# Optimization experiments

Measured on AMD Instinct MI355X. Metric: run time of the kernel, lower is better.

The kernel has to match this reference:

```python
import jax, jax.numpy as jnp
import numpy as np

N_NODES = 2_000_000
N_EDGES = 16_777_216
N_REL = 4


def setup_inputs() -> dict:
    key = jax.random.key(0)
    ks = jax.random.split(key, 13)
    inp = {
        "author_x": jax.random.normal(ks[0], (N_NODES, 4), jnp.float32),
        "paper_x": jax.random.normal(ks[1], (N_NODES, 4), jnp.float32),
        "src_index": jax.random.randint(ks[2], (N_EDGES,), 0, N_NODES, jnp.int64 if jax.config.jax_enable_x64 else jnp.int32).astype(jnp.int32),
        "dst_index": jax.random.randint(ks[3], (N_EDGES,), 0, N_NODES).astype(jnp.int32),
        "edge_type_index": jax.random.randint(ks[4], (N_EDGES,), 0, N_REL).astype(jnp.int32),
        "edge_src_is_paper": jax.random.randint(ks[5], (N_REL,), 0, 2).astype(jnp.int32),
        "edge_dst_is_paper": jax.random.randint(ks[6], (N_REL,), 0, 2).astype(jnp.int32),
        "Wa": jax.random.normal(ks[7], (4, 4), jnp.float32) * 0.5,
        "ba": jax.random.normal(ks[8], (4,), jnp.float32) * 0.1,
        "Wp": jax.random.normal(ks[9], (4, 4), jnp.float32) * 0.5,
        "bp": jax.random.normal(ks[10], (4,), jnp.float32) * 0.1,
        "Ws": jax.random.normal(ks[11], (8,), jnp.float32) * 0.5,
        "bs": jax.random.normal(ks[12], (1,), jnp.float32) * 0.1,
    }
    return inp


def reference(author_x, paper_x, src_index, dst_index, edge_type_index,
              edge_src_is_paper, edge_dst_is_paper, Wa, ba, Wp, bp, Ws, bs):
    # Encode node tables (tiny GEMMs): [N,4] @ [4,4]^T + [4]
    author_h = author_x @ Wa.T + ba
    paper_h = paper_x @ Wp.T + bp
    # Per-edge relation-type dispatch: 1 = paper table, 0 = author table
    src_p = edge_src_is_paper[edge_type_index].astype(bool)  # [E]
    dst_p = edge_dst_is_paper[edge_type_index].astype(bool)  # [E]
    src_repr = jnp.where(src_p[:, None], paper_h[src_index], author_h[src_index])  # [E,4]
    dst_repr = jnp.where(dst_p[:, None], paper_h[dst_index], author_h[dst_index])  # [E,4]
    # scorer: Linear(8,1) on concat, squeeze last dim -> [E]
    logits = jnp.concatenate([src_repr, dst_repr], axis=-1) @ Ws + bs[0]
    return logits
```

## Files before the change

kernel.cpp:

```cpp
#include <hip/hip_runtime.h>

typedef int         iv4 __attribute__((ext_vector_type(4)));
typedef float       fv4 __attribute__((ext_vector_type(4)));
typedef _Float16    hv4 __attribute__((ext_vector_type(4)));

struct Fold {
    float va_s[4], va_d[4], vp_s[4], vp_d[4];
    float ca_s, ca_d, cp_s, cp_d;
};

__device__ inline Fold make_fold(const float* __restrict__ Wa, const float* __restrict__ ba,
                                 const float* __restrict__ Wp, const float* __restrict__ bp,
                                 const float* __restrict__ Ws) {
    Fold f;
    float w0 = Ws[0], w1 = Ws[1], w2 = Ws[2], w3 = Ws[3];
    float w4 = Ws[4], w5 = Ws[5], w6 = Ws[6], w7 = Ws[7];
#pragma unroll
    for (int j = 0; j < 4; ++j) {
        f.va_s[j] = w0*Wa[j] + w1*Wa[4+j] + w2*Wa[8+j] + w3*Wa[12+j];
        f.va_d[j] = w4*Wa[j] + w5*Wa[4+j] + w6*Wa[8+j] + w7*Wa[12+j];
        f.vp_s[j] = w0*Wp[j] + w1*Wp[4+j] + w2*Wp[8+j] + w3*Wp[12+j];
        f.vp_d[j] = w4*Wp[j] + w5*Wp[4+j] + w6*Wp[8+j] + w7*Wp[12+j];
    }
    f.ca_s = w0*ba[0] + w1*ba[1] + w2*ba[2] + w3*ba[3];
    f.ca_d = w4*ba[0] + w5*ba[1] + w6*ba[2] + w7*ba[3];
    f.cp_s = w0*bp[0] + w1*bp[1] + w2*bp[2] + w3*bp[3];
    f.cp_d = w4*bp[0] + w5*bp[1] + w6*bp[2] + w7*bp[3];
    return f;
}

__device__ inline void node_scores(const Fold& f, fv4 a, fv4 p,
                                   float& as, float& ps, float& ad, float& pd) {
    as = a.x*f.va_s[0] + a.y*f.va_s[1] + a.z*f.va_s[2] + a.w*f.va_s[3] + f.ca_s;
    ad = a.x*f.va_d[0] + a.y*f.va_d[1] + a.z*f.va_d[2] + a.w*f.va_d[3] + f.ca_d;
    ps = p.x*f.vp_s[0] + p.y*f.vp_s[1] + p.z*f.vp_s[2] + p.w*f.vp_s[3] + f.cp_s;
    pd = p.x*f.vp_d[0] + p.y*f.vp_d[1] + p.z*f.vp_d[2] + p.w*f.vp_d[3] + f.cp_d;
}

__global__ __launch_bounds__(256) void node_pass1(
    const fv4* __restrict__ ax, const fv4* __restrict__ px,
    const float* __restrict__ Wa, const float* __restrict__ ba,
    const float* __restrict__ Wp, const float* __restrict__ bp,
    const float* __restrict__ Ws,
    hv4* __restrict__ sc, unsigned* __restrict__ maxes, int n)
{
    Fold f = make_fold(Wa, ba, Wp, bp, Ws);
    float ms = 0.f, md = 0.f;
    int stride = gridDim.x * blockDim.x;
    for (int i = blockIdx.x * blockDim.x + threadIdx.x; i < n; i += stride) {
        fv4 a = __builtin_nontemporal_load(ax + i);
        fv4 p = __builtin_nontemporal_load(px + i);
        float as, ps, ad, pd;
        node_scores(f, a, p, as, ps, ad, pd);
        hv4 h;
        h.x = (_Float16)as; h.y = (_Float16)ps; h.z = (_Float16)ad; h.w = (_Float16)pd;
        sc[i] = h;
        ms = fmaxf(ms, fmaxf(fabsf(as), fabsf(ps)));
        md = fmaxf(md, fmaxf(fabsf(ad), fabsf(pd)));
    }
#pragma unroll
    for (int off = 32; off >= 1; off >>= 1) {
        ms = fmaxf(ms, __shfl_down(ms, off));
        md = fmaxf(md, __shfl_down(md, off));
    }
    __shared__ float lms[4], lmd[4];
    int wave = threadIdx.x >> 6, lane = threadIdx.x & 63;
    if (lane == 0) { lms[wave] = ms; lmd[wave] = md; }
    __syncthreads();
    if (threadIdx.x == 0) {
        float bms = fmaxf(fmaxf(lms[0], lms[1]), fmaxf(lms[2], lms[3]));
        float bmd = fmaxf(fmaxf(lmd[0], lmd[1]), fmaxf(lmd[2], lmd[3]));
        atomicMax(&maxes[0], __float_as_uint(bms));
        atomicMax(&maxes[1], __float_as_uint(bmd));
    }
}

__global__ __launch_bounds__(256) void node_pass2(
    const hv4* __restrict__ sc, const unsigned* __restrict__ maxes,
    unsigned long long* __restrict__ ts8, unsigned long long* __restrict__ td8, int n4)
{
    int i = blockIdx.x * blockDim.x + threadIdx.x;
    if (i >= n4) return;
    float inv_s = 127.f / fmaxf(__uint_as_float(maxes[0]), 1e-20f);
    float inv_d = 127.f / fmaxf(__uint_as_float(maxes[1]), 1e-20f);
    unsigned long long vs = 0, vd = 0;
#pragma unroll
    for (int j = 0; j < 4; ++j) {
        hv4 h = sc[4*i + j];
        int qas = min(127, max(-127, __float2int_rn((float)h.x * inv_s)));
        int qps = min(127, max(-127, __float2int_rn((float)h.y * inv_s)));
        int qad = min(127, max(-127, __float2int_rn((float)h.z * inv_d)));
        int qpd = min(127, max(-127, __float2int_rn((float)h.w * inv_d)));
        vs |= (unsigned long long)((unsigned)qas & 0xffu) << (16*j);
        vs |= (unsigned long long)((unsigned)qps & 0xffu) << (16*j + 8);
        vd |= (unsigned long long)((unsigned)qad & 0xffu) << (16*j);
        vd |= (unsigned long long)((unsigned)qpd & 0xffu) << (16*j + 8);
    }
    ts8[i] = vs;
    td8[i] = vd;
}

__global__ __launch_bounds__(256) void edge_src_pass(
    const iv4* __restrict__ src4, const iv4* __restrict__ et4,
    const int* __restrict__ esp, const int* __restrict__ edp,
    const signed char* __restrict__ ts,
    unsigned long long* __restrict__ qsrc,
    unsigned char* __restrict__ dbits, int n8)
{
    int i = blockIdx.x * blockDim.x + threadIdx.x;
    if (i >= n8) return;
    unsigned smask = (unsigned)((esp[0]&1) | ((esp[1]&1)<<1) | ((esp[2]&1)<<2) | ((esp[3]&1)<<3));
    unsigned dmask = (unsigned)((edp[0]&1) | ((edp[1]&1)<<1) | ((edp[2]&1)<<2) | ((edp[3]&1)<<3));

    iv4 s0 = __builtin_nontemporal_load(src4 + 2*i);
    iv4 s1 = __builtin_nontemporal_load(src4 + 2*i + 1);
    iv4 t0 = __builtin_nontemporal_load(et4 + 2*i);
    iv4 t1 = __builtin_nontemporal_load(et4 + 2*i + 1);
    int ty[8] = { t0.x&3, t0.y&3, t0.z&3, t0.w&3, t1.x&3, t1.y&3, t1.z&3, t1.w&3 };
    int sx[8] = { s0.x, s0.y, s0.z, s0.w, s1.x, s1.y, s1.z, s1.w };

    int a[8];
#pragma unroll
    for (int k = 0; k < 8; ++k) a[k] = 2*sx[k] + (int)((smask >> ty[k]) & 1u);

    int q[8];
#pragma unroll
    for (int k = 0; k < 8; ++k) q[k] = (int)ts[a[k]];

    unsigned long long o = 0;
    unsigned db = 0;
#pragma unroll
    for (int k = 0; k < 8; ++k) {
        o |= (unsigned long long)((unsigned)q[k] & 0xffu) << (8*k);
        db |= ((dmask >> ty[k]) & 1u) << k;
    }
    __builtin_nontemporal_store(o, qsrc + i);
    __builtin_nontemporal_store((unsigned char)db, dbits + i);
}

__global__ __launch_bounds__(256) void edge_dst_pass(
    const iv4* __restrict__ dst4,
    const unsigned char* __restrict__ dbits,
    const float* __restrict__ bs, const unsigned* __restrict__ maxes,
    const signed char* __restrict__ td,
    const unsigned long long* __restrict__ qsrc,
    fv4* __restrict__ out4, int n8)
{
    int i = blockIdx.x * blockDim.x + threadIdx.x;
    if (i >= n8) return;
    float b = bs[0];
    float scale_s = __uint_as_float(maxes[0]) * (1.f / 127.f);
    float scale_d = __uint_as_float(maxes[1]) * (1.f / 127.f);

    iv4 d0 = __builtin_nontemporal_load(dst4 + 2*i);
    iv4 d1 = __builtin_nontemporal_load(dst4 + 2*i + 1);
    unsigned db = (unsigned)dbits[i];
    unsigned long long qq = qsrc[i];
    int dx[8] = { d0.x, d0.y, d0.z, d0.w, d1.x, d1.y, d1.z, d1.w };

    int a[8];
#pragma unroll
    for (int k = 0; k < 8; ++k) a[k] = 2*dx[k] + (int)((db >> k) & 1u);

    int qd[8];
#pragma unroll
    for (int k = 0; k < 8; ++k) qd[k] = (int)td[a[k]];

    float r[8];
#pragma unroll
    for (int k = 0; k < 8; ++k) {
        int qs = (int)(signed char)((qq >> (8*k)) & 0xffull);
        r[k] = (float)qs * scale_s + (float)qd[k] * scale_d + b;
    }
    fv4 o0, o1;
    o0.x = r[0]; o0.y = r[1]; o0.z = r[2]; o0.w = r[3];
    o1.x = r[4]; o1.y = r[5]; o1.z = r[6]; o1.w = r[7];
    __builtin_nontemporal_store(o0, out4 + 2*i);
    __builtin_nontemporal_store(o1, out4 + 2*i + 1);
}

__global__ __launch_bounds__(256) void fused_kernel(
    const fv4* __restrict__ ax, const fv4* __restrict__ px,
    const int* __restrict__ src, const int* __restrict__ dst, const int* __restrict__ et,
    const int* __restrict__ esp, const int* __restrict__ edp,
    const float* __restrict__ Wa, const float* __restrict__ ba,
    const float* __restrict__ Wp, const float* __restrict__ bp,
    const float* __restrict__ Ws, const float* __restrict__ bs,
    float* __restrict__ out, int n)
{
    int e = blockIdx.x * blockDim.x + threadIdx.x;
    if (e >= n) return;
    Fold f = make_fold(Wa, ba, Wp, bp, Ws);
    int t = et[e];
    int sp = esp[t] & 1, dp = edp[t] & 1;
    fv4 sv = sp ? px[src[e]] : ax[src[e]];
    fv4 dv = dp ? px[dst[e]] : ax[dst[e]];
    float ssc = sp ? (sv.x*f.vp_s[0] + sv.y*f.vp_s[1] + sv.z*f.vp_s[2] + sv.w*f.vp_s[3] + f.cp_s)
                   : (sv.x*f.va_s[0] + sv.y*f.va_s[1] + sv.z*f.va_s[2] + sv.w*f.va_s[3] + f.ca_s);
    float dsc = dp ? (dv.x*f.vp_d[0] + dv.y*f.vp_d[1] + dv.z*f.vp_d[2] + dv.w*f.vp_d[3] + f.cp_d)
                   : (dv.x*f.va_d[0] + dv.y*f.va_d[1] + dv.z*f.va_d[2] + dv.w*f.va_d[3] + f.ca_d);
    out[e] = ssc + dsc + bs[0];
}

extern "C" void kernel_launch(void* const* d_in, const int* in_sizes, int n_in,
                              void* d_out, int out_size, void* d_ws, size_t ws_size,
                              hipStream_t stream) {
    const float* ax  = (const float*)d_in[0];
    const float* px  = (const float*)d_in[1];
    const int*   src = (const int*)d_in[2];
    const int*   dst = (const int*)d_in[3];
    const int*   et  = (const int*)d_in[4];
    const int*   esp = (const int*)d_in[5];
    const int*   edp = (const int*)d_in[6];
    const float* Wa  = (const float*)d_in[7];
    const float* ba  = (const float*)d_in[8];
    const float* Wp  = (const float*)d_in[9];
    const float* bp  = (const float*)d_in[10];
    const float* Ws  = (const float*)d_in[11];
    const float* bs  = (const float*)d_in[12];
    float* out = (float*)d_out;

    const int n_nodes = in_sizes[0] / 4;
    const int n_edges = in_sizes[2];

    auto rnd = [](size_t v) { return (v + 255) & ~(size_t)255; };
    size_t union_sz = rnd((size_t)n_edges > (size_t)n_nodes * 8 ? (size_t)n_edges
                                                                : (size_t)n_nodes * 8);
    const size_t off_u  = 256;
    const size_t off_ts = off_u + union_sz;
    const size_t off_td = off_ts + rnd((size_t)n_nodes * 2);
    const size_t off_db = off_td + rnd((size_t)n_nodes * 2);
    const size_t need   = off_db + rnd((size_t)(n_edges / 8) + 1);

    if (ws_size >= need && (n_edges & 7) == 0 && (n_nodes & 3) == 0) {
        unsigned* maxes = (unsigned*)d_ws;
        hv4* sc = (hv4*)((char*)d_ws + off_u);
        unsigned long long* qsrc = (unsigned long long*)((char*)d_ws + off_u);
        signed char* ts = (signed char*)((char*)d_ws + off_ts);
        signed char* td = (signed char*)((char*)d_ws + off_td);
        unsigned char* dbits = (unsigned char*)((char*)d_ws + off_db);

        (void)hipMemsetAsync(maxes, 0, 2 * sizeof(unsigned), stream);
        node_pass1<<<2048, 256, 0, stream>>>(
            (const fv4*)ax, (const fv4*)px, Wa, ba, Wp, bp, Ws, sc, maxes, n_nodes);
        const int n4 = n_nodes / 4;
        node_pass2<<<(n4 + 255) / 256, 256, 0, stream>>>(
            sc, maxes, (unsigned long long*)ts, (unsigned long long*)td, n4);

        const int n8 = n_edges / 8;
        const int nb = (n8 + 255) / 256;
        edge_src_pass<<<nb, 256, 0, stream>>>(
            (const iv4*)src, (const iv4*)et, esp, edp, ts, qsrc, dbits, n8);
        edge_dst_pass<<<nb, 256, 0, stream>>>(
            (const iv4*)dst, dbits, bs, maxes, td, qsrc, (fv4*)out, n8);
    } else {
        fused_kernel<<<(n_edges + 255) / 256, 256, 0, stream>>>(
            (const fv4*)ax, (const fv4*)px, src, dst, et, esp, edp,
            Wa, ba, Wp, bp, Ws, bs, out, n_edges);
    }
}
```

Before: 460.1 us.

## Recompute node scores in pass2 instead of staging fp16 intermediates; drop atomics and memset

Pass1 now only computes per-block abs-max values and writes them to a small array, with no fp16 score buffer. Pass2 reduces those block maxima inside every block and recomputes the node scores from the raw inputs before quantizing. This removes the 16 MB fp16 write and read, the memset launch and the global atomics. In exchange the 64 MB node input is read twice, and every pass2 block redundantly reduces 2048 partial maxima.

```diff
diff --git a/kernel.cpp b/kernel.cpp
--- a/kernel.cpp
+++ b/kernel.cpp
@@ -2,7 +2,6 @@
 
 typedef int         iv4 __attribute__((ext_vector_type(4)));
 typedef float       fv4 __attribute__((ext_vector_type(4)));
-typedef _Float16    hv4 __attribute__((ext_vector_type(4)));
 
 struct Fold {
     float va_s[4], va_d[4], vp_s[4], vp_d[4];
@@ -37,24 +36,23 @@
     pd = p.x*f.vp_d[0] + p.y*f.vp_d[1] + p.z*f.vp_d[2] + p.w*f.vp_d[3] + f.cp_d;
 }
 
+#define P1_BLOCKS 2048
+
 __global__ __launch_bounds__(256) void node_pass1(
     const fv4* __restrict__ ax, const fv4* __restrict__ px,
     const float* __restrict__ Wa, const float* __restrict__ ba,
     const float* __restrict__ Wp, const float* __restrict__ bp,
     const float* __restrict__ Ws,
-    hv4* __restrict__ sc, unsigned* __restrict__ maxes, int n)
+    float* __restrict__ bms, float* __restrict__ bmd, int n)
 {
     Fold f = make_fold(Wa, ba, Wp, bp, Ws);
     float ms = 0.f, md = 0.f;
     int stride = gridDim.x * blockDim.x;
     for (int i = blockIdx.x * blockDim.x + threadIdx.x; i < n; i += stride) {
-        fv4 a = __builtin_nontemporal_load(ax + i);
-        fv4 p = __builtin_nontemporal_load(px + i);
+        fv4 a = ax[i];
+        fv4 p = px[i];
         float as, ps, ad, pd;
         node_scores(f, a, p, as, ps, ad, pd);
-        hv4 h;
-        h.x = (_Float16)as; h.y = (_Float16)ps; h.z = (_Float16)ad; h.w = (_Float16)pd;
-        sc[i] = h;
         ms = fmaxf(ms, fmaxf(fabsf(as), fabsf(ps)));
         md = fmaxf(md, fmaxf(fabsf(ad), fabsf(pd)));
     }
@@ -68,29 +66,58 @@
     if (lane == 0) { lms[wave] = ms; lmd[wave] = md; }
     __syncthreads();
     if (threadIdx.x == 0) {
-        float bms = fmaxf(fmaxf(lms[0], lms[1]), fmaxf(lms[2], lms[3]));
-        float bmd = fmaxf(fmaxf(lmd[0], lmd[1]), fmaxf(lmd[2], lmd[3]));
-        atomicMax(&maxes[0], __float_as_uint(bms));
-        atomicMax(&maxes[1], __float_as_uint(bmd));
+        bms[blockIdx.x] = fmaxf(fmaxf(lms[0], lms[1]), fmaxf(lms[2], lms[3]));
+        bmd[blockIdx.x] = fmaxf(fmaxf(lmd[0], lmd[1]), fmaxf(lmd[2], lmd[3]));
     }
 }
 
 __global__ __launch_bounds__(256) void node_pass2(
-    const hv4* __restrict__ sc, const unsigned* __restrict__ maxes,
+    const fv4* __restrict__ ax, const fv4* __restrict__ px,
+    const float* __restrict__ Wa, const float* __restrict__ ba,
+    const float* __restrict__ Wp, const float* __restrict__ bp,
+    const float* __restrict__ Ws,
+    const float* __restrict__ bms, const float* __restrict__ bmd, int nblk,
+    float* __restrict__ maxf,
     unsigned long long* __restrict__ ts8, unsigned long long* __restrict__ td8, int n4)
 {
+    float ms = 0.f, md = 0.f;
+    for (int j = threadIdx.x; j < nblk; j += 256) {
+        ms = fmaxf(ms, bms[j]);
+        md = fmaxf(md, bmd[j]);
+    }
+#pragma unroll
+    for (int off = 32; off >= 1; off >>= 1) {
+        ms = fmaxf(ms, __shfl_down(ms, off));
+        md = fmaxf(md, __shfl_down(md, off));
+    }
+    __shared__ float lms[4], lmd[4], fin[2];
+    int wave = threadIdx.x >> 6, lane = threadIdx.x & 63;
+    if (lane == 0) { lms[wave] = ms; lmd[wave] = md; }
+    __syncthreads();
+    if (threadIdx.x == 0) {
+        float gs = fmaxf(fmaxf(lms[0], lms[1]), fmaxf(lms[2], lms[3]));
+        float gd = fmaxf(fmaxf(lmd[0], lmd[1]), fmaxf(lmd[2], lmd[3]));
+        fin[0] = gs; fin[1] = gd;
+        if (blockIdx.x == 0) { maxf[0] = gs; maxf[1] = gd; }
+    }
+    __syncthreads();
+    float inv_s = 127.f / fmaxf(fin[0], 1e-20f);
+    float inv_d = 127.f / fmaxf(fin[1], 1e-20f);
+
     int i = blockIdx.x * blockDim.x + threadIdx.x;
     if (i >= n4) return;
-    float inv_s = 127.f / fmaxf(__uint_as_float(maxes[0]), 1e-20f);
-    float inv_d = 127.f / fmaxf(__uint_as_float(maxes[1]), 1e-20f);
+    Fold f = make_fold(Wa, ba, Wp, bp, Ws);
     unsigned long long vs = 0, vd = 0;
 #pragma unroll
     for (int j = 0; j < 4; ++j) {
-        hv4 h = sc[4*i + j];
-        int qas = min(127, max(-127, __float2int_rn((float)h.x * inv_s)));
-        int qps = min(127, max(-127, __float2int_rn((float)h.y * inv_s)));
-        int qad = min(127, max(-127, __float2int_rn((float)h.z * inv_d)));
-        int qpd = min(127, max(-127, __float2int_rn((float)h.w * inv_d)));
+        fv4 a = ax[4*i + j];
+        fv4 p = px[4*i + j];
+        float as, ps, ad, pd;
+        node_scores(f, a, p, as, ps, ad, pd);
+        int qas = min(127, max(-127, __float2int_rn(as * inv_s)));
+        int qps = min(127, max(-127, __float2int_rn(ps * inv_s)));
+        int qad = min(127, max(-127, __float2int_rn(ad * inv_d)));
+        int qpd = min(127, max(-127, __float2int_rn(pd * inv_d)));
         vs |= (unsigned long long)((unsigned)qas & 0xffu) << (16*j);
         vs |= (unsigned long long)((unsigned)qps & 0xffu) << (16*j + 8);
         vd |= (unsigned long long)((unsigned)qad & 0xffu) << (16*j);
@@ -141,7 +168,7 @@
 __global__ __launch_bounds__(256) void edge_dst_pass(
     const iv4* __restrict__ dst4,
     const unsigned char* __restrict__ dbits,
-    const float* __restrict__ bs, const unsigned* __restrict__ maxes,
+    const float* __restrict__ bs, const float* __restrict__ maxf,
     const signed char* __restrict__ td,
     const unsigned long long* __restrict__ qsrc,
     fv4* __restrict__ out4, int n8)
@@ -149,8 +176,8 @@
     int i = blockIdx.x * blockDim.x + threadIdx.x;
     if (i >= n8) return;
     float b = bs[0];
-    float scale_s = __uint_as_float(maxes[0]) * (1.f / 127.f);
-    float scale_d = __uint_as_float(maxes[1]) * (1.f / 127.f);
+    float scale_s = maxf[0] * (1.f / 127.f);
+    float scale_d = maxf[1] * (1.f / 127.f);
 
     iv4 d0 = __builtin_nontemporal_load(dst4 + 2*i);
     iv4 d1 = __builtin_nontemporal_load(dst4 + 2*i + 1);
@@ -224,35 +251,38 @@
     const int n_edges = in_sizes[2];
 
     auto rnd = [](size_t v) { return (v + 255) & ~(size_t)255; };
-    size_t union_sz = rnd((size_t)n_edges > (size_t)n_nodes * 8 ? (size_t)n_edges
-                                                                : (size_t)n_nodes * 8);
-    const size_t off_u  = 256;
-    const size_t off_ts = off_u + union_sz;
-    const size_t off_td = off_ts + rnd((size_t)n_nodes * 2);
-    const size_t off_db = off_td + rnd((size_t)n_nodes * 2);
-    const size_t need   = off_db + rnd((size_t)(n_edges / 8) + 1);
+    const size_t off_bms = 0;
+    const size_t off_bmd = off_bms + rnd((size_t)P1_BLOCKS * 4);
+    const size_t off_mx  = off_bmd + rnd((size_t)P1_BLOCKS * 4);
+    const size_t off_q   = off_mx + 256;
+    const size_t off_ts  = off_q + rnd((size_t)n_edges);
+    const size_t off_td  = off_ts + rnd((size_t)n_nodes * 2);
+    const size_t off_db  = off_td + rnd((size_t)n_nodes * 2);
+    const size_t need    = off_db + rnd((size_t)(n_edges / 8) + 1);
 
     if (ws_size >= need && (n_edges & 7) == 0 && (n_nodes & 3) == 0) {
-        unsigned* maxes = (unsigned*)d_ws;
-        hv4* sc = (hv4*)((char*)d_ws + off_u);
-        unsigned long long* qsrc = (unsigned long long*)((char*)d_ws + off_u);
+        float* bms = (float*)((char*)d_ws + off_bms);
+        float* bmd = (float*)((char*)d_ws + off_bmd);
+        float* maxf = (float*)((char*)d_ws + off_mx);
+        unsigned long long* qsrc = (unsigned long long*)((char*)d_ws + off_q);
         signed char* ts = (signed char*)((char*)d_ws + off_ts);
         signed char* td = (signed char*)((char*)d_ws + off_td);
         unsigned char* dbits = (unsigned char*)((char*)d_ws + off_db);
 
-        (void)hipMemsetAsync(maxes, 0, 2 * sizeof(unsigned), stream);
-        node_pass1<<<2048, 256, 0, stream>>>(
-            (const fv4*)ax, (const fv4*)px, Wa, ba, Wp, bp, Ws, sc, maxes, n_nodes);
+        node_pass1<<<P1_BLOCKS, 256, 0, stream>>>(
+            (const fv4*)ax, (const fv4*)px, Wa, ba, Wp, bp, Ws, bms, bmd, n_nodes);
         const int n4 = n_nodes / 4;
         node_pass2<<<(n4 + 255) / 256, 256, 0, stream>>>(
-            sc, maxes, (unsigned long long*)ts, (unsigned long long*)td, n4);
+            (const fv4*)ax, (const fv4*)px, Wa, ba, Wp, bp, Ws,
+            bms, bmd, P1_BLOCKS, maxf,
+            (unsigned long long*)ts, (unsigned long long*)td, n4);
 
         const int n8 = n_edges / 8;
         const int nb = (n8 + 255) / 256;
         edge_src_pass<<<nb, 256, 0, stream>>>(
             (const iv4*)src, (const iv4*)et, esp, edp, ts, qsrc, dbits, n8);
         edge_dst_pass<<<nb, 256, 0, stream>>>(
-            (const iv4*)dst, dbits, bs, maxes, td, qsrc, (fv4*)out, n8);
+            (const iv4*)dst, dbits, bs, maxf, td, qsrc, (fv4*)out, n8);
     } else {
         fused_kernel<<<(n_edges + 255) / 256, 256, 0, stream>>>(
             (const fv4*)ax, (const fv4*)px, src, dst, et, esp, edp,
```

After: 433.7 us, median of 2. 5.7% less time.
